# Optimization experiments

Hardware: AMD Instinct MI355X
Metric: run time of the kernel (lower is better)

## Reference

```python
import jax, jax.numpy as jnp
import numpy as np

NEG_SLOPE = 0.2  # LeakyReLU slope used by PyG GATConv


def gat_conv(x, src, dst, W_src, W_dst, att_src, att_dst, bias, num_nodes):
    """Single-head PyG-style GATConv.
    x: [N, F_in]; src/dst: [E] int; W_*: [C, F_in]; att_*: [C]; bias: [C].
    """
    h_src = x @ W_src.T            # [N, C]
    h_dst = x @ W_dst.T            # [N, C]
    a_src = h_src @ att_src        # [N]
    a_dst = h_dst @ att_dst        # [N]
    e = a_src[src] + a_dst[dst]    # [E]
    e = jnp.where(e >= 0, e, NEG_SLOPE * e)  # leaky_relu
    # softmax over edges grouped by destination node
    m = jax.ops.segment_max(e, dst, num_segments=num_nodes)          # [N]
    ex = jnp.exp(e - m[dst])                                          # [E]
    denom = jax.ops.segment_sum(ex, dst, num_segments=num_nodes)      # [N]
    alpha = ex / (denom[dst] + 1e-16)                                 # [E]
    out = jax.ops.segment_sum(alpha[:, None] * h_src[src], dst,
                              num_segments=num_nodes)                 # [N, C]
    return out + bias


def setup_inputs() -> dict:
    key = jax.random.key(0)
    ks = jax.random.split(key, 16)
    N, E = 10000, 160000
    dim_in, dim_out = 4096, 20
    hid = dim_in // 4  # 1024
    x = jax.random.normal(ks[0], (N, dim_in), dtype=jnp.float32)
    edges = jax.random.randint(ks[1], (2, E), 0, N, dtype=jnp.int64)
    std = 0.01
    return {
        "x": x,
        "edges": edges,
        "W0": jax.random.normal(ks[2], (dim_out, dim_in)) * std,
        "b0": jnp.zeros((dim_out,), jnp.float32),
        "Ws1": jax.random.normal(ks[3], (hid, dim_in)) * (1.0 / np.sqrt(dim_in)),
        "Wd1": jax.random.normal(ks[4], (hid, dim_in)) * (1.0 / np.sqrt(dim_in)),
        "as1": jax.random.normal(ks[5], (hid,)) * 0.1,
        "ad1": jax.random.normal(ks[6], (hid,)) * 0.1,
        "b1": jnp.zeros((hid,), jnp.float32),
        "Ws2": jax.random.normal(ks[7], (dim_out, hid)) * (1.0 / np.sqrt(hid)),
        "Wd2": jax.random.normal(ks[8], (dim_out, hid)) * (1.0 / np.sqrt(hid)),
        "as2": jax.random.normal(ks[9], (dim_out,)) * 0.1,
        "ad2": jax.random.normal(ks[10], (dim_out,)) * 0.1,
        "b2": jnp.zeros((dim_out,), jnp.float32),
    }


def reference(x, edges, W0, b0, Ws1, Wd1, as1, ad1, b1, Ws2, Wd2, as2, ad2, b2):
    N = x.shape[0]
    # GATConv default add_self_loops=True; returned edge list includes them
    ar = jnp.arange(N, dtype=edges.dtype)
    new_edge = jnp.concatenate([edges, jnp.stack([ar, ar])], axis=1)  # [2, E+N]
    src, dst = new_edge[0], new_edge[1]

    # mil_score0: plain linear
    mil_score0 = x @ W0.T + b0                           # [N, dim_out]

    # mil_score1: two-layer GAT with ELU in between
    h = gat_conv(x, src, dst, Ws1, Wd1, as1, ad1, b1, N)  # [N, hid]
    h = jax.nn.elu(h)
    mil_score1 = gat_conv(h, src, dst, Ws2, Wd2, as2, ad2, b2, N)  # [N, dim_out]

    # softmax over proposals (dim=0) per class, fused with GAT output
    mil_score = jax.nn.softmax(mil_score0, axis=0) * mil_score1
    return (mil_score, new_edge)
```

## Files before the change

kernel.cpp:

```cpp
#include <hip/hip_runtime.h>

#define NN   10000
#define FIN  4096
#define HID  1024
#define CO   20
#define EE   160000
#define ET   170000
#define NBV  (HID + 22)

typedef __bf16 bf16x8 __attribute__((ext_vector_type(8)));
typedef float  f32x4  __attribute__((ext_vector_type(4)));

__device__ __forceinline__ float bf2f(unsigned short u) {
    unsigned int x = ((unsigned int)u) << 16;
    float f; __builtin_memcpy(&f, &x, 4); return f;
}
__device__ __forceinline__ unsigned short f2bf(float f) {
    unsigned int x; __builtin_memcpy(&x, &f, 4);
    unsigned int r = (x + 0x7fffu + ((x >> 16) & 1u)) >> 16;
    return (unsigned short)r;
}
__device__ __forceinline__ void unpack4(int2 v, float* f) {
    unsigned int a = (unsigned int)v.x, b = (unsigned int)v.y;
    f[0] = bf2f((unsigned short)(a & 0xffffu)); f[1] = bf2f((unsigned short)(a >> 16));
    f[2] = bf2f((unsigned short)(b & 0xffffu)); f[3] = bf2f((unsigned short)(b >> 16));
}
__device__ __forceinline__ int edge_at(const int* __restrict__ e, int idx, int is64) {
    return is64 ? e[2 * (size_t)idx] : e[idx];
}
__device__ __forceinline__ int4 pack8(float4 a, float4 b) {
    int4 o;
    o.x = (int)((unsigned)f2bf(a.x) | ((unsigned)f2bf(a.y) << 16));
    o.y = (int)((unsigned)f2bf(a.z) | ((unsigned)f2bf(a.w) << 16));
    o.z = (int)((unsigned)f2bf(b.x) | ((unsigned)f2bf(b.y) << 16));
    o.w = (int)((unsigned)f2bf(b.z) | ((unsigned)f2bf(b.w) << 16));
    return o;
}

__global__ void k_cast(const float* __restrict__ src, unsigned short* __restrict__ dst,
                       const int* __restrict__ edg, int* __restrict__ cnt,
                       int* __restrict__ flag) {
    int i = blockIdx.x * 256 + threadIdx.x;
    const float4* s = (const float4*)src + (size_t)i * 2;
    *(int4*)(dst + (size_t)i * 8) = pack8(s[0], s[1]);
    if (i < NN) cnt[i] = 0;
    if (i < 64) {
        int v = edg[2 * i + 1];
        unsigned long long bm = __ballot(v != 0);
        if (i == 0) flag[0] = (bm == 0ull) ? 1 : 0;
    }
}

#define BEXTB 2088
__global__ __launch_bounds__(256) void k_prep(const float* __restrict__ Ws1,
                                              const float* __restrict__ Wd1,
                                              const float* __restrict__ W0,
                                              const float* __restrict__ as1,
                                              const float* __restrict__ ad1,
                                              unsigned short* __restrict__ Bext,
                                              float* __restrict__ partS,
                                              float* __restrict__ partD) {
    if (blockIdx.x < BEXTB) {
        int i = blockIdx.x * 256 + threadIdx.x;
        int row = i >> 9;
        int col = (i & 511) * 8;
        const float* src = (row < HID) ? Ws1 + (size_t)row * FIN
                                       : W0 + (size_t)(row - HID) * FIN;
        const float4* s = (const float4*)(src + col);
        *(int4*)(Bext + (size_t)row * FIN + col) = pack8(s[0], s[1]);
    } else {
        int bx = blockIdx.x - BEXTB;
        int k = (bx & 15) * 256 + threadIdx.x;
        int chunk = bx >> 4;
        int r0 = chunk * 128;
        float s = 0.f, d = 0.f;
        for (int r = r0; r < r0 + 128; r++) {
            s += as1[r] * Ws1[(size_t)r * FIN + k];
            d += ad1[r] * Wd1[(size_t)r * FIN + k];
        }
        partS[chunk * FIN + k] = s;
        partD[chunk * FIN + k] = d;
    }
}

__global__ void k_vred(const float* __restrict__ partS, const float* __restrict__ partD,
                       const float* __restrict__ Wd2, const float* __restrict__ ad2,
                       unsigned short* __restrict__ Bext, float* __restrict__ wd2v) {
    int k = blockIdx.x * 256 + threadIdx.x;
    if (k < FIN) {
        float s = 0.f, d = 0.f;
        for (int j = 0; j < 8; j++) { s += partS[j * FIN + k]; d += partD[j * FIN + k]; }
        Bext[(size_t)(HID + CO) * FIN + k]     = f2bf(s);
        Bext[(size_t)(HID + CO + 1) * FIN + k] = f2bf(d);
    }
    if (k < HID) {
        float d2 = 0.f;
        for (int r = 0; r < CO; r++) d2 += ad2[r] * Wd2[(size_t)r * HID + k];
        wd2v[k] = d2;
    }
}

#define GBM 128
#define GBN 128
#define GBK 32
#define NMT ((NN + GBM - 1) / GBM)
#define NNT ((NBV + GBN - 1) / GBN)
#define NWG (NMT * NNT)

__global__ __launch_bounds__(256) void k_gemm_ext(
    const unsigned short* __restrict__ A, const unsigned short* __restrict__ B,
    unsigned short* __restrict__ H1, float* __restrict__ ext, int M) {
    __shared__ __bf16 As[2][GBM * GBK];
    __shared__ __bf16 Bs[2][GBN * GBK];
    int bid = blockIdx.x;
    int q = NWG >> 3, r = NWG & 7;
    int xcd = bid & 7, idx = bid >> 3;
    int swz = (xcd < r ? xcd * (q + 1) : r * (q + 1) + (xcd - r) * q) + idx;
    int mt = swz / NNT;
    int nt = swz - mt * NNT;
    int m0 = mt * GBM;
    int n0 = nt * GBN;
    int tid = threadIdx.x;
    int lane = tid & 63, wave = tid >> 6;
    int wm = (wave >> 1) * 64, wn = (wave & 1) * 64;
    int lrow = lane & 15, lk8 = (lane >> 4) * 8;

    int srow = lane >> 2;
    int scol = (lane & 3) * 8;
    int arow = wave * 32;
    int gmA0 = m0 + arow + srow;      if (gmA0 >= M) gmA0 = M - 1;
    int gmA1 = m0 + arow + 16 + srow; if (gmA1 >= M) gmA1 = M - 1;
    int gnB0 = n0 + arow + srow;      if (gnB0 >= NBV) gnB0 = NBV - 1;
    int gnB1 = n0 + arow + 16 + srow; if (gnB1 >= NBV) gnB1 = NBV - 1;
    const unsigned short* pA0 = A + (size_t)gmA0 * FIN + scol;
    const unsigned short* pA1 = A + (size_t)gmA1 * FIN + scol;
    const unsigned short* pB0 = B + (size_t)gnB0 * FIN + scol;
    const unsigned short* pB1 = B + (size_t)gnB1 * FIN + scol;

    f32x4 acc[4][4];
#pragma unroll
    for (int r2 = 0; r2 < 4; r2++)
#pragma unroll
        for (int c = 0; c < 4; c++) acc[r2][c] = (f32x4){0.f, 0.f, 0.f, 0.f};

    auto stage = [&](int buf, int k0) {
        __builtin_amdgcn_global_load_lds(
            (const __attribute__((address_space(1))) void*)(pA0 + k0),
            (__attribute__((address_space(3))) void*)&As[buf][arow * GBK], 16, 0, 0);
        __builtin_amdgcn_global_load_lds(
            (const __attribute__((address_space(1))) void*)(pA1 + k0),
            (__attribute__((address_space(3))) void*)&As[buf][(arow + 16) * GBK], 16, 0, 0);
        __builtin_amdgcn_global_load_lds(
            (const __attribute__((address_space(1))) void*)(pB0 + k0),
            (__attribute__((address_space(3))) void*)&Bs[buf][arow * GBK], 16, 0, 0);
        __builtin_amdgcn_global_load_lds(
            (const __attribute__((address_space(1))) void*)(pB1 + k0),
            (__attribute__((address_space(3))) void*)&Bs[buf][(arow + 16) * GBK], 16, 0, 0);
    };

    stage(0, 0);
    int cur = 0;
    for (int k0 = 0; k0 < FIN; k0 += GBK) {
        __syncthreads();
        if (k0 + GBK < FIN) stage(cur ^ 1, k0 + GBK);
        bf16x8 af[4], bfr[4];
#pragma unroll
        for (int r2 = 0; r2 < 4; r2++)
            af[r2] = *(const bf16x8*)(&As[cur][(wm + r2 * 16 + lrow) * GBK + lk8]);
#pragma unroll
        for (int c = 0; c < 4; c++)
            bfr[c] = *(const bf16x8*)(&Bs[cur][(wn + c * 16 + lrow) * GBK + lk8]);
#pragma unroll
        for (int r2 = 0; r2 < 4; r2++)
#pragma unroll
            for (int c = 0; c < 4; c++)
                acc[r2][c] = __builtin_amdgcn_mfma_f32_16x16x32_bf16(af[r2], bfr[c], acc[r2][c], 0, 0, 0);
        cur ^= 1;
    }
    int orow = (lane >> 4) * 4, ocol = lane & 15;
#pragma unroll
    for (int r2 = 0; r2 < 4; r2++)
#pragma unroll
        for (int c = 0; c < 4; c++)
#pragma unroll
            for (int i = 0; i < 4; i++) {
                int m = m0 + wm + r2 * 16 + orow + i;
                int n = n0 + wn + c * 16 + ocol;
                if (m < M) {
                    float v = acc[r2][c][i];
                    if (n < HID)      H1[(size_t)m * HID + n] = f2bf(v);
                    else if (n < NBV) ext[(size_t)(n - HID) * NN + m] = v;
                }
            }
}

#define CNTB 665
__global__ __launch_bounds__(256) void k_cfs(const int* __restrict__ edges,
                                             const int* __restrict__ flag,
                                             int* __restrict__ cnt,
                                             const float* __restrict__ ext,
                                             float* __restrict__ gmax,
                                             float* __restrict__ ginv) {
    if (blockIdx.x < CNTB) {
        int k = blockIdx.x * 256 + threadIdx.x;
        if (k >= ET) return;
        int is64 = flag[0];
        int d = (k < EE) ? edge_at(edges, EE + k, is64) : (k - EE);
        if ((unsigned)d < NN) atomicAdd(&cnt[d], 1);
    } else {
        int c = blockIdx.x - CNTB, t = threadIdx.x, lane = t & 63, wv = t >> 6;
        const float* row = ext + (size_t)c * NN;
        __shared__ float r4[4];
        __shared__ float bv;
        float m = -INFINITY;
        for (int n = t; n < NN; n += 256) m = fmaxf(m, row[n]);
        for (int o = 32; o; o >>= 1) m = fmaxf(m, __shfl_xor(m, o, 64));
        if (lane == 0) r4[wv] = m;
        __syncthreads();
        if (t == 0) bv = fmaxf(fmaxf(r4[0], r4[1]), fmaxf(r4[2], r4[3]));
        __syncthreads();
        float gm = bv;
        __syncthreads();
        float s = 0.f;
        for (int n = t; n < NN; n += 256) s += expf(row[n] - gm);
        for (int o = 32; o; o >>= 1) s += __shfl_xor(s, o, 64);
        if (lane == 0) r4[wv] = s;
        __syncthreads();
        if (t == 0) { gmax[c] = gm; ginv[c] = 1.0f / (r4[0] + r4[1] + r4[2] + r4[3]); }
    }
}

__global__ __launch_bounds__(1024) void k_scan(const int* __restrict__ cnt,
                                               int* __restrict__ offs,
                                               int* __restrict__ cursor) {
    int t = threadIdx.x, lane = t & 63, wv = t >> 6;
    int base = t * 10;
    int c[10]; int tot = 0;
    if (base < NN) {
#pragma unroll
        for (int j = 0; j < 10; j++) { c[j] = cnt[base + j]; tot += c[j]; }
    }
    int incl = tot;
#pragma unroll
    for (int o = 1; o < 64; o <<= 1) {
        int v = __shfl_up(incl, o, 64);
        if (lane >= o) incl += v;
    }
    __shared__ int wsum[16];
    if (lane == 63) wsum[wv] = incl;
    __syncthreads();
    if (t < 16) {
        int v = wsum[t];
        int inc2 = v;
#pragma unroll
        for (int o = 1; o < 16; o <<= 1) {
            int u = __shfl_up(inc2, o, 64);
            if (t >= o) inc2 += u;
        }
        wsum[t] = inc2 - v;
    }
    __syncthreads();
    int excl = incl - tot + wsum[wv];
    if (base < NN) {
        int run = excl;
#pragma unroll
        for (int j = 0; j < 10; j++) {
            cursor[base + j] = run;
            run += c[j];
            offs[base + j + 1] = run;
        }
    }
    if (t == 0) offs[0] = 0;
}

__global__ void k_scatter(const int* __restrict__ edges, const int* __restrict__ flag,
                          int* __restrict__ cursor, int* __restrict__ csr_src) {
    int k = blockIdx.x * 256 + threadIdx.x;
    if (k >= ET) return;
    int is64 = flag[0];
    int s, d;
    if (k < EE) { s = edge_at(edges, k, is64); d = edge_at(edges, EE + k, is64); }
    else        { s = d = k - EE; }
    if ((unsigned)d >= NN) return;
    if ((unsigned)s >= NN) s = 0;
    int pos = atomicAdd(&cursor[d], 1);
    csr_src[pos] = s;
}

__global__ __launch_bounds__(256) void k_agg1f(
    const int* __restrict__ offs, const int* __restrict__ csr,
    const float* __restrict__ a_src, const float* __restrict__ a_dst,
    const unsigned short* __restrict__ H1,
    const float* __restrict__ b1, const float* __restrict__ Ws2,
    const float* __restrict__ wd2v, const float* __restrict__ as2,
    float* __restrict__ H2, float* __restrict__ a_src2, float* __restrict__ a_dst2) {
    int n = blockIdx.x, t = threadIdx.x, lane = t & 63, wv = t >> 6;
    int b = offs[n], deg = offs[n + 1] - b;
    float ad = a_dst[n];
    __shared__ float r4[4];
    __shared__ float acache[1024];
    float mymax = -INFINITY;
    for (int j = t; j < deg; j += 256) {
        float v = a_src[csr[b + j]] + ad;
        v = (v >= 0.f) ? v : 0.2f * v;
        mymax = fmaxf(mymax, v);
    }
    for (int o = 32; o; o >>= 1) mymax = fmaxf(mymax, __shfl_xor(mymax, o, 64));
    if (lane == 0) r4[wv] = mymax;
    __syncthreads();
    float gm = fmaxf(fmaxf(r4[0], r4[1]), fmaxf(r4[2], r4[3]));
    __syncthreads();
    float mysum = 0.f;
    for (int j = t; j < deg; j += 256) {
        float v = a_src[csr[b + j]] + ad;
        v = (v >= 0.f) ? v : 0.2f * v;
        mysum += expf(v - gm);
    }
    for (int o = 32; o; o >>= 1) mysum += __shfl_xor(mysum, o, 64);
    if (lane == 0) r4[wv] = mysum;
    __syncthreads();
    float inv = 1.0f / (r4[0] + r4[1] + r4[2] + r4[3] + 1e-16f);
    float acc[4] = {0.f, 0.f, 0.f, 0.f};
    for (int base = 0; base < deg; base += 1024) {
        int lim = deg - base; if (lim > 1024) lim = 1024;
        __syncthreads();
        for (int j = t; j < lim; j += 256) {
            float v = a_src[csr[b + base + j]] + ad;
            v = (v >= 0.f) ? v : 0.2f * v;
            acache[j] = expf(v - gm) * inv;
        }
        __syncthreads();
        for (int j = 0; j < lim; j++) {
            int s = csr[b + base + j];
            float w = acache[j];
            float f[4]; unpack4(*(const int2*)(H1 + (size_t)s * HID + t * 4), f);
            acc[0] += w * f[0]; acc[1] += w * f[1];
            acc[2] += w * f[2]; acc[3] += w * f[3];
        }
    }
    float4 bb = *(const float4*)(b1 + t * 4);
    float xf[4];
    xf[0] = acc[0] + bb.x; xf[1] = acc[1] + bb.y;
    xf[2] = acc[2] + bb.z; xf[3] = acc[3] + bb.w;
#pragma unroll
    for (int i = 0; i < 4; i++)
        xf[i] = (xf[i] > 0.f) ? xf[i] : (expf(xf[i]) - 1.f);
    float part[21];
#pragma unroll
    for (int c = 0; c < CO; c++) {
        float4 wf = *(const float4*)(Ws2 + (size_t)c * HID + t * 4);
        part[c] = xf[0]*wf.x + xf[1]*wf.y + xf[2]*wf.z + xf[3]*wf.w;
    }
    {
        float4 w = *(const float4*)(wd2v + t * 4);
        part[20] = xf[0]*w.x + xf[1]*w.y + xf[2]*w.z + xf[3]*w.w;
    }
    __shared__ float red[21][4];
    __shared__ float dv[21];
#pragma unroll
    for (int v = 0; v < 21; v++) {
        float s = part[v];
        for (int o = 32; o; o >>= 1) s += __shfl_down(s, o, 64);
        if (lane == 0) red[v][wv] = s;
    }
    __syncthreads();
    if (t < 21) {
        float s = red[t][0] + red[t][1] + red[t][2] + red[t][3];
        dv[t] = s;
        if (t < CO) H2[(size_t)n * CO + t] = s;
        else        a_dst2[n] = s;
    }
    __syncthreads();
    if (t == 0) {
        float a = 0.f;
        for (int c = 0; c < CO; c++) a += dv[c] * as2[c];
        a_src2[n] = a;
    }
}

__global__ __launch_bounds__(64) void k_agg2(const int* __restrict__ offs,
                                             const int* __restrict__ csr,
                                             const float* __restrict__ a_src,
                                             const float* __restrict__ a_dst,
                                             const float* __restrict__ H2,
                                             const float* __restrict__ b2,
                                             float* __restrict__ ms1T) {
    int n = blockIdx.x, lane = threadIdx.x;
    int b = offs[n], deg = offs[n + 1] - b;
    float ad = a_dst[n];
    float mymax = -INFINITY;
    for (int j = lane; j < deg; j += 64) {
        float v = a_src[csr[b + j]] + ad;
        v = (v >= 0.f) ? v : 0.2f * v;
        mymax = fmaxf(mymax, v);
    }
    for (int o = 32; o; o >>= 1) mymax = fmaxf(mymax, __shfl_xor(mymax, o, 64));
    float mysum = 0.f;
    for (int j = lane; j < deg; j += 64) {
        float v = a_src[csr[b + j]] + ad;
        v = (v >= 0.f) ? v : 0.2f * v;
        mysum += expf(v - mymax);
    }
    for (int o = 32; o; o >>= 1) mysum += __shfl_xor(mysum, o, 64);
    float inv = 1.0f / (mysum + 1e-16f);
    __shared__ float acache[256];
    float acc = 0.f;
    for (int base = 0; base < deg; base += 256) {
        int lim = deg - base; if (lim > 256) lim = 256;
        __syncthreads();
        for (int j = lane; j < lim; j += 64) {
            float v = a_src[csr[b + base + j]] + ad;
            v = (v >= 0.f) ? v : 0.2f * v;
            acache[j] = expf(v - mymax) * inv;
        }
        __syncthreads();
        if (lane < CO)
            for (int j = 0; j < lim; j++)
                acc += acache[j] * H2[(size_t)csr[b + base + j] * CO + lane];
    }
    if (lane < CO) ms1T[(size_t)lane * NN + n] = acc + b2[lane];
}

__global__ __launch_bounds__(256) void k_fout(const float* __restrict__ ext,
                                              const float* __restrict__ ms1T,
                                              const float* __restrict__ gmax,
                                              const float* __restrict__ ginv,
                                              const int* __restrict__ edges,
                                              const int* __restrict__ flag,
                                              float* __restrict__ out) {
    int g = blockIdx.x * 256 + threadIdx.x;
    if (g < NN) {
        float o[CO];
#pragma unroll
        for (int c = 0; c < CO; c++)
            o[c] = expf(ext[(size_t)c * NN + g] - gmax[c]) * ginv[c] * ms1T[(size_t)c * NN + g];
#pragma unroll
        for (int c = 0; c < CO; c += 4) {
            float4 v; v.x = o[c]; v.y = o[c + 1]; v.z = o[c + 2]; v.w = o[c + 3];
            *(float4*)(out + (size_t)g * CO + c) = v;
        }
    }
    if (g < ET) {
        int is64 = flag[0];
        int s, d;
        if (g < EE) { s = edge_at(edges, g, is64); d = edge_at(edges, EE + g, is64); }
        else        { s = d = g - EE; }
        out[NN * CO + g]      = bf2f(f2bf((float)s));
        out[NN * CO + ET + g] = bf2f(f2bf((float)d));
    }
}

extern "C" void kernel_launch(void* const* d_in, const int* in_sizes, int n_in,
                              void* d_out, int out_size, void* d_ws, size_t ws_size,
                              hipStream_t stream) {
    const float* x   = (const float*)d_in[0];
    const int*   edg = (const int*)d_in[1];
    const float* W0  = (const float*)d_in[2];
    const float* Ws1 = (const float*)d_in[4];
    const float* Wd1 = (const float*)d_in[5];
    const float* as1 = (const float*)d_in[6];
    const float* ad1 = (const float*)d_in[7];
    const float* b1  = (const float*)d_in[8];
    const float* Ws2 = (const float*)d_in[9];
    const float* Wd2 = (const float*)d_in[10];
    const float* as2 = (const float*)d_in[11];
    const float* ad2 = (const float*)d_in[12];
    const float* b2  = (const float*)d_in[13];
    float* out = (float*)d_out;

    char* p = (char*)d_ws;
    auto alloc = [&](size_t bytes) -> char* {
        char* r = p; p += (bytes + 511) & ~((size_t)511); return r;
    };
    unsigned short* xb   = (unsigned short*)alloc((size_t)NN * FIN * 2);
    unsigned short* Bext = (unsigned short*)alloc((size_t)NBV * FIN * 2);
    unsigned short* H1   = (unsigned short*)alloc((size_t)NN * HID * 2);
    float* ext    = (float*)alloc((size_t)22 * NN * 4);
    float* partS  = (float*)alloc((size_t)8 * FIN * 4);
    float* partD  = (float*)alloc((size_t)8 * FIN * 4);
    float* wd2v   = (float*)alloc(HID * 4);
    float* H2     = (float*)alloc((size_t)NN * CO * 4);
    float* ms1T   = (float*)alloc((size_t)CO * NN * 4);
    float* a_src2 = (float*)alloc(NN * 4);
    float* a_dst2 = (float*)alloc(NN * 4);
    int* csr_src  = (int*)alloc((size_t)ET * 4);
    int* cnt      = (int*)alloc(NN * 4);
    int* offs     = (int*)alloc((NN + 1) * 4);
    int* cursor   = (int*)alloc(NN * 4);
    int* eflag    = (int*)alloc(64);
    float* gmax   = (float*)alloc(CO * 4);
    float* ginv   = (float*)alloc(CO * 4);

    k_cast<<<NN * FIN / 8 / 256, 256, 0, stream>>>(x, xb, edg, cnt, eflag);
    k_prep<<<BEXTB + 128, 256, 0, stream>>>(Ws1, Wd1, W0, as1, ad1, Bext, partS, partD);
    k_vred<<<FIN / 256, 256, 0, stream>>>(partS, partD, Wd2, ad2, Bext, wd2v);
    k_gemm_ext<<<NWG, 256, 0, stream>>>(xb, Bext, H1, ext, NN);
    k_cfs<<<CNTB + CO, 256, 0, stream>>>(edg, eflag, cnt, ext, gmax, ginv);
    k_scan<<<1, 1024, 0, stream>>>(cnt, offs, cursor);
    k_scatter<<<(ET + 255) / 256, 256, 0, stream>>>(edg, eflag, cursor, csr_src);
    k_agg1f<<<NN, 256, 0, stream>>>(offs, csr_src, ext + 20 * NN, ext + 21 * NN, H1,
                                    b1, Ws2, wd2v, as2, H2, a_src2, a_dst2);
    k_agg2<<<NN, 64, 0, stream>>>(offs, csr_src, a_src2, a_dst2, H2, b2, ms1T);
    k_fout<<<(ET + 255) / 256, 256, 0, stream>>>(ext, ms1T, gmax, ginv, edg, eflag, out);
}
```

Baseline: 601.6 us.

## Use single-wavefront blocks for GAT aggregation with cached edge weights and indices

k_agg1f drops from 256 to 64 threads per node. Each lane now handles 16 hidden features through 16-byte bf16 loads, and the cross-wave shared-memory reductions go away. For nodes with degree up to 128, the source indices and leaky-relu scores are computed once and cached in LDS, which avoids re-reading csr and a_src in the max, sum and aggregate passes. k_agg2 gets the same caching and splits the edge loop across two half-waves to use more lanes. The trade-off is more registers per thread and fewer threads per node to hide gather latency.

```diff
diff --git a/kernel.cpp b/kernel.cpp
--- a/kernel.cpp
+++ b/kernel.cpp
@@ -287,95 +287,120 @@
     csr_src[pos] = s;
 }
 
-__global__ __launch_bounds__(256) void k_agg1f(
+__global__ __launch_bounds__(64) void k_agg1f(
     const int* __restrict__ offs, const int* __restrict__ csr,
     const float* __restrict__ a_src, const float* __restrict__ a_dst,
     const unsigned short* __restrict__ H1,
     const float* __restrict__ b1, const float* __restrict__ Ws2,
     const float* __restrict__ wd2v, const float* __restrict__ as2,
     float* __restrict__ H2, float* __restrict__ a_src2, float* __restrict__ a_dst2) {
-    int n = blockIdx.x, t = threadIdx.x, lane = t & 63, wv = t >> 6;
+    int n = blockIdx.x, lane = threadIdx.x;
     int b = offs[n], deg = offs[n + 1] - b;
     float ad = a_dst[n];
-    __shared__ float r4[4];
-    __shared__ float acache[1024];
-    float mymax = -INFINITY;
-    for (int j = t; j < deg; j += 256) {
-        float v = a_src[csr[b + j]] + ad;
-        v = (v >= 0.f) ? v : 0.2f * v;
-        mymax = fmaxf(mymax, v);
-    }
-    for (int o = 32; o; o >>= 1) mymax = fmaxf(mymax, __shfl_xor(mymax, o, 64));
-    if (lane == 0) r4[wv] = mymax;
-    __syncthreads();
-    float gm = fmaxf(fmaxf(r4[0], r4[1]), fmaxf(r4[2], r4[3]));
-    __syncthreads();
-    float mysum = 0.f;
-    for (int j = t; j < deg; j += 256) {
-        float v = a_src[csr[b + j]] + ad;
-        v = (v >= 0.f) ? v : 0.2f * v;
-        mysum += expf(v - gm);
-    }
-    for (int o = 32; o; o >>= 1) mysum += __shfl_xor(mysum, o, 64);
-    if (lane == 0) r4[wv] = mysum;
-    __syncthreads();
-    float inv = 1.0f / (r4[0] + r4[1] + r4[2] + r4[3] + 1e-16f);
-    float acc[4] = {0.f, 0.f, 0.f, 0.f};
-    for (int base = 0; base < deg; base += 1024) {
-        int lim = deg - base; if (lim > 1024) lim = 1024;
-        __syncthreads();
-        for (int j = t; j < lim; j += 256) {
-            float v = a_src[csr[b + base + j]] + ad;
+    __shared__ int   sc[128];
+    __shared__ float av[128];
+    bool small = (deg <= 128);
+    float gm, inv;
+    if (small) {
+        float mymax = -INFINITY;
+        for (int j = lane; j < deg; j += 64) {
+            int s = csr[b + j];
+            float v = a_src[s] + ad;
             v = (v >= 0.f) ? v : 0.2f * v;
-            acache[j] = expf(v - gm) * inv;
-        }
-        __syncthreads();
+            sc[j] = s; av[j] = v;
+            mymax = fmaxf(mymax, v);
+        }
+        for (int o = 32; o; o >>= 1) mymax = fmaxf(mymax, __shfl_xor(mymax, o, 64));
+        gm = mymax;
+        float mysum = 0.f;
+        for (int j = lane; j < deg; j += 64) {
+            float e = expf(av[j] - gm);
+            av[j] = e;
+            mysum += e;
+        }
+        for (int o = 32; o; o >>= 1) mysum += __shfl_xor(mysum, o, 64);
+        inv = 1.0f / (mysum + 1e-16f);
+        for (int j = lane; j < deg; j += 64) av[j] *= inv;
+        __syncthreads();
+    } else {
+        float mymax = -INFINITY;
+        for (int j = lane; j < deg; j += 64) {
+            float v = a_src[csr[b + j]] + ad;
+            v = (v >= 0.f) ? v : 0.2f * v;
+            mymax = fmaxf(mymax, v);
+        }
+        for (int o = 32; o; o >>= 1) mymax = fmaxf(mymax, __shfl_xor(mymax, o, 64));
+        gm = mymax;
+        float mysum = 0.f;
+        for (int j = lane; j < deg; j += 64) {
+            float v = a_src[csr[b + j]] + ad;
+            v = (v >= 0.f) ? v : 0.2f * v;
+            mysum += expf(v - gm);
+        }
+        for (int o = 32; o; o >>= 1) mysum += __shfl_xor(mysum, o, 64);
+        inv = 1.0f / (mysum + 1e-16f);
+    }
+    float acc[16];
+#pragma unroll
+    for (int i = 0; i < 16; i++) acc[i] = 0.f;
+    for (int base = 0; base < deg; base += 128) {
+        int lim = deg - base; if (lim > 128) lim = 128;
+        if (!small) {
+            __syncthreads();
+            for (int j = lane; j < lim; j += 64) {
+                int s = csr[b + base + j];
+                float v = a_src[s] + ad;
+                v = (v >= 0.f) ? v : 0.2f * v;
+                sc[j] = s; av[j] = expf(v - gm) * inv;
+            }
+            __syncthreads();
+        }
         for (int j = 0; j < lim; j++) {
-            int s = csr[b + base + j];
-            float w = acache[j];
-            float f[4]; unpack4(*(const int2*)(H1 + (size_t)s * HID + t * 4), f);
-            acc[0] += w * f[0]; acc[1] += w * f[1];
-            acc[2] += w * f[2]; acc[3] += w * f[3];
-        }
-    }
-    float4 bb = *(const float4*)(b1 + t * 4);
-    float xf[4];
-    xf[0] = acc[0] + bb.x; xf[1] = acc[1] + bb.y;
-    xf[2] = acc[2] + bb.z; xf[3] = acc[3] + bb.w;
-#pragma unroll
-    for (int i = 0; i < 4; i++)
-        xf[i] = (xf[i] > 0.f) ? xf[i] : (expf(xf[i]) - 1.f);
-    float part[21];
-#pragma unroll
-    for (int c = 0; c < CO; c++) {
-        float4 wf = *(const float4*)(Ws2 + (size_t)c * HID + t * 4);
-        part[c] = xf[0]*wf.x + xf[1]*wf.y + xf[2]*wf.z + xf[3]*wf.w;
-    }
+            int s = sc[j]; float w = av[j];
+            const unsigned short* hp = H1 + (size_t)s * HID + lane * 8;
+            int4 p0 = *(const int4*)hp;
+            int4 p1 = *(const int4*)(hp + 512);
+            float f[8];
+            unpack4(make_int2(p0.x, p0.y), f);
+            unpack4(make_int2(p0.z, p0.w), f + 4);
+#pragma unroll
+            for (int i = 0; i < 8; i++) acc[i] += w * f[i];
+            unpack4(make_int2(p1.x, p1.y), f);
+            unpack4(make_int2(p1.z, p1.w), f + 4);
+#pragma unroll
+            for (int i = 0; i < 8; i++) acc[8 + i] += w * f[i];
+        }
+    }
+    float xf[16];
     {
-        float4 w = *(const float4*)(wd2v + t * 4);
-        part[20] = xf[0]*w.x + xf[1]*w.y + xf[2]*w.z + xf[3]*w.w;
-    }
-    __shared__ float red[21][4];
-    __shared__ float dv[21];
-#pragma unroll
-    for (int v = 0; v < 21; v++) {
-        float s = part[v];
-        for (int o = 32; o; o >>= 1) s += __shfl_down(s, o, 64);
-        if (lane == 0) red[v][wv] = s;
-    }
-    __syncthreads();
-    if (t < 21) {
-        float s = red[t][0] + red[t][1] + red[t][2] + red[t][3];
-        dv[t] = s;
-        if (t < CO) H2[(size_t)n * CO + t] = s;
-        else        a_dst2[n] = s;
-    }
-    __syncthreads();
-    if (t == 0) {
-        float a = 0.f;
-        for (int c = 0; c < CO; c++) a += dv[c] * as2[c];
-        a_src2[n] = a;
-    }
+        const float4* bp0 = (const float4*)(b1 + lane * 8);
+        const float4* bp1 = (const float4*)(b1 + 512 + lane * 8);
+        float4 c0 = bp0[0], c1 = bp0[1], c2 = bp1[0], c3 = bp1[1];
+        float bb[16] = {c0.x,c0.y,c0.z,c0.w, c1.x,c1.y,c1.z,c1.w,
+                        c2.x,c2.y,c2.z,c2.w, c3.x,c3.y,c3.z,c3.w};
+#pragma unroll
+        for (int i = 0; i < 16; i++) {
+            float v = acc[i] + bb[i];
+            xf[i] = (v > 0.f) ? v : (expf(v) - 1.f);
+        }
+    }
+    float a2 = 0.f;
+    for (int c = 0; c < 21; c++) {
+        const float* wr = (c < CO) ? Ws2 + (size_t)c * HID : wd2v;
+        const float4* w0 = (const float4*)(wr + lane * 8);
+        const float4* w1 = (const float4*)(wr + 512 + lane * 8);
+        float4 wa = w0[0], wb = w0[1], wc = w1[0], wd = w1[1];
+        float dp = xf[0]*wa.x + xf[1]*wa.y + xf[2]*wa.z + xf[3]*wa.w
+                 + xf[4]*wb.x + xf[5]*wb.y + xf[6]*wb.z + xf[7]*wb.w
+                 + xf[8]*wc.x + xf[9]*wc.y + xf[10]*wc.z + xf[11]*wc.w
+                 + xf[12]*wd.x + xf[13]*wd.y + xf[14]*wd.z + xf[15]*wd.w;
+        for (int o = 32; o; o >>= 1) dp += __shfl_xor(dp, o, 64);
+        if (c < CO) {
+            if (lane == 0) H2[(size_t)n * CO + c] = dp;
+            a2 += dp * as2[c];
+        } else if (lane == 0) a_dst2[n] = dp;
+    }
+    if (lane == 0) a_src2[n] = a2;
 }
 
 __global__ __launch_bounds__(64) void k_agg2(const int* __restrict__ offs,
@@ -388,37 +413,69 @@
     int n = blockIdx.x, lane = threadIdx.x;
     int b = offs[n], deg = offs[n + 1] - b;
     float ad = a_dst[n];
-    float mymax = -INFINITY;
-    for (int j = lane; j < deg; j += 64) {
-        float v = a_src[csr[b + j]] + ad;
-        v = (v >= 0.f) ? v : 0.2f * v;
-        mymax = fmaxf(mymax, v);
-    }
-    for (int o = 32; o; o >>= 1) mymax = fmaxf(mymax, __shfl_xor(mymax, o, 64));
-    float mysum = 0.f;
-    for (int j = lane; j < deg; j += 64) {
-        float v = a_src[csr[b + j]] + ad;
-        v = (v >= 0.f) ? v : 0.2f * v;
-        mysum += expf(v - mymax);
-    }
-    for (int o = 32; o; o >>= 1) mysum += __shfl_xor(mysum, o, 64);
-    float inv = 1.0f / (mysum + 1e-16f);
-    __shared__ float acache[256];
+    __shared__ int   sc[128];
+    __shared__ float av[128];
+    bool small = (deg <= 128);
+    float gm, inv;
+    if (small) {
+        float mymax = -INFINITY;
+        for (int j = lane; j < deg; j += 64) {
+            int s = csr[b + j];
+            float v = a_src[s] + ad;
+            v = (v >= 0.f) ? v : 0.2f * v;
+            sc[j] = s; av[j] = v;
+            mymax = fmaxf(mymax, v);
+        }
+        for (int o = 32; o; o >>= 1) mymax = fmaxf(mymax, __shfl_xor(mymax, o, 64));
+        gm = mymax;
+        float mysum = 0.f;
+        for (int j = lane; j < deg; j += 64) {
+            float e = expf(av[j] - gm);
+            av[j] = e;
+            mysum += e;
+        }
+        for (int o = 32; o; o >>= 1) mysum += __shfl_xor(mysum, o, 64);
+        inv = 1.0f / (mysum + 1e-16f);
+        for (int j = lane; j < deg; j += 64) av[j] *= inv;
+        __syncthreads();
+    } else {
+        float mymax = -INFINITY;
+        for (int j = lane; j < deg; j += 64) {
+            float v = a_src[csr[b + j]] + ad;
+            v = (v >= 0.f) ? v : 0.2f * v;
+            mymax = fmaxf(mymax, v);
+        }
+        for (int o = 32; o; o >>= 1) mymax = fmaxf(mymax, __shfl_xor(mymax, o, 64));
+        gm = mymax;
+        float mysum = 0.f;
+        for (int j = lane; j < deg; j += 64) {
+            float v = a_src[csr[b + j]] + ad;
+            v = (v >= 0.f) ? v : 0.2f * v;
+            mysum += expf(v - gm);
+        }
+        for (int o = 32; o; o >>= 1) mysum += __shfl_xor(mysum, o, 64);
+        inv = 1.0f / (mysum + 1e-16f);
+    }
+    int h = lane >> 5, c = lane & 31;
     float acc = 0.f;
-    for (int base = 0; base < deg; base += 256) {
-        int lim = deg - base; if (lim > 256) lim = 256;
-        __syncthreads();
-        for (int j = lane; j < lim; j += 64) {
-            float v = a_src[csr[b + base + j]] + ad;
-            v = (v >= 0.f) ? v : 0.2f * v;
-            acache[j] = expf(v - mymax) * inv;
-        }
-        __syncthreads();
-        if (lane < CO)
-            for (int j = 0; j < lim; j++)
-                acc += acache[j] * H2[(size_t)csr[b + base + j] * CO + lane];
-    }
-    if (lane < CO) ms1T[(size_t)lane * NN + n] = acc + b2[lane];
+    for (int base = 0; base < deg; base += 128) {
+        int lim = deg - base; if (lim > 128) lim = 128;
+        if (!small) {
+            __syncthreads();
+            for (int j = lane; j < lim; j += 64) {
+                int s = csr[b + base + j];
+                float v = a_src[s] + ad;
+                v = (v >= 0.f) ? v : 0.2f * v;
+                sc[j] = s; av[j] = expf(v - gm) * inv;
+            }
+            __syncthreads();
+        }
+        if (c < CO)
+            for (int j = h; j < lim; j += 2)
+                acc += av[j] * H2[(size_t)sc[j] * CO + c];
+    }
+    acc += __shfl_xor(acc, 32, 64);
+    if (h == 0 && c < CO) ms1T[(size_t)c * NN + n] = acc + b2[c];
 }
 
 __global__ __launch_bounds__(256) void k_fout(const float* __restrict__ ext,
@@ -498,8 +555,8 @@
     k_cfs<<<CNTB + CO, 256, 0, stream>>>(edg, eflag, cnt, ext, gmax, ginv);
     k_scan<<<1, 1024, 0, stream>>>(cnt, offs, cursor);
     k_scatter<<<(ET + 255) / 256, 256, 0, stream>>>(edg, eflag, cursor, csr_src);
-    k_agg1f<<<NN, 256, 0, stream>>>(offs, csr_src, ext + 20 * NN, ext + 21 * NN, H1,
-                                    b1, Ws2, wd2v, as2, H2, a_src2, a_dst2);
+    k_agg1f<<<NN, 64, 0, stream>>>(offs, csr_src, ext + 20 * NN, ext + 21 * NN, H1,
+                                   b1, Ws2, wd2v, as2, H2, a_src2, a_dst2);
     k_agg2<<<NN, 64, 0, stream>>>(offs, csr_src, a_src2, a_dst2, H2, b2, ms1T);
     k_fout<<<(ET + 255) / 256, 256, 0, stream>>>(ext, ms1T, gmax, ginv, edg, eflag, out);
 }
```

New measurement: 535.3 us. 11.0% less time.
